# Performance work log

Measured on AMD Instinct MI355X. Metric: run time of the kernel, lower is better.

The kernel has to match this reference:

```python
import jax, jax.numpy as jnp
import numpy as np
from jax.scipy.linalg import expm

U_SHAPE = (4, 32, 16, 16, 16, 3, 3)   # [mu, t, x, y, z, 3, 3]
W_SHAPE = (8, 32, 16, 16, 16, 3, 3)   # [feature, t, x, y, z, 3, 3]


def setup_inputs() -> dict:
    key = jax.random.key(0)
    k = jax.random.split(key, 5)
    return {
        "U_re": jax.random.normal(k[0], U_SHAPE, jnp.float32),
        "U_im": jax.random.normal(k[1], U_SHAPE, jnp.float32),
        "W_re": jax.random.normal(k[2], W_SHAPE, jnp.float32),
        "W_im": jax.random.normal(k[3], W_SHAPE, jnp.float32),
        "ah_weights": jax.random.normal(k[4], (4, W_SHAPE[0]), jnp.float32),
    }


def reference(U_re, U_im, W_re, W_im, ah_weights):
    U = (U_re + 1j * U_im).astype(jnp.complex64)
    W = (W_re + 1j * W_im).astype(jnp.complex64)

    # anti-hermitian part: W - W^dagger
    W_adj = jnp.conj(jnp.swapaxes(W, -1, -2))
    A = W - W_adj
    # traceless projection
    tr = jnp.trace(A, axis1=-2, axis2=-1)  # [i,t,x,y,z]
    A = A - (tr / 3.0)[..., None, None] * jnp.eye(3, dtype=A.dtype)

    # exponent: (1j*w) contracted with (-1j*A) == w contracted with A
    E = jnp.einsum('ui,itxyzab->utxyzab', ah_weights.astype(A.dtype), A)

    # batched 3x3 matrix exponential over the whole lattice
    E_flat = E.reshape(-1, 3, 3)
    expE = jax.vmap(expm)(E_flat).reshape(E.shape)

    # apply to gauge links: exp(...) @ U
    return jnp.einsum('utxyzij,utxyzjk->utxyzik', expE, U)
```

## Files before the change

kernel.cpp:

```cpp
#include <hip/hip_runtime.h>
#include <math.h>

#define NSITES 131072

struct cplx { float re, im; };

__device__ __forceinline__ cplx cadd(cplx a, cplx b) { return {a.re + b.re, a.im + b.im}; }
__device__ __forceinline__ cplx csub(cplx a, cplx b) { return {a.re - b.re, a.im - b.im}; }
__device__ __forceinline__ cplx cmul(cplx a, cplx b) {
    return { fmaf(a.re, b.re, -(a.im * b.im)), fmaf(a.re, b.im, a.im * b.re) };
}
__device__ __forceinline__ cplx cmadd(cplx a, cplx b, cplx c) {
    return { fmaf(a.re, b.re, fmaf(-a.im, b.im, c.re)),
             fmaf(a.re, b.im, fmaf( a.im, b.re, c.im)) };
}
__device__ __forceinline__ cplx cscale(cplx a, float s) { return {a.re * s, a.im * s}; }

struct __attribute__((aligned(4))) f3 { float x, y, z; };
__device__ __forceinline__ void ld9(const float* __restrict__ p, float* r) {
    f3 a = *(const f3*)p, b = *(const f3*)(p + 3), c = *(const f3*)(p + 6);
    r[0] = a.x; r[1] = a.y; r[2] = a.z;
    r[3] = b.x; r[4] = b.y; r[5] = b.z;
    r[6] = c.x; r[7] = c.y; r[8] = c.z;
}

#define GLDS(g, l) __builtin_amdgcn_global_load_lds( \
    (const __attribute__((address_space(1))) void*)(g), \
    (__attribute__((address_space(3))) void*)(l), 16, 0, 0)

__global__ __launch_bounds__(256, 4) void lge_exp_kernel(
    const float* __restrict__ U_re, const float* __restrict__ U_im,
    const float* __restrict__ W_re, const float* __restrict__ W_im,
    const float* __restrict__ ahw,  float* __restrict__ out)
{
    __shared__ __align__(16) float Wl[4 * 2304];

    const int tid   = threadIdx.x;
    const int w     = tid >> 6;
    const int lane  = tid & 63;
    const int site0 = blockIdx.x << 6;

    {
        const char* baseRe = (const char*)W_re;
        const char* baseIm = (const char*)W_im;
        float* ldst = Wl + w * 2304 + ((16 * 64) / 4) * 0;
        #pragma unroll
        for (int k = 0; k < 9; k++) {
            int p   = k * 64 + lane;
            int c   = p / 36;
            int off = (p - c * 36) * 16;
            int f   = c & 7;
            const char* gb = (c < 8) ? baseRe : baseIm;
            const char* g  = gb + (size_t)((f * NSITES + site0 + 16 * w)) * 36 + off;
            GLDS(g, (char*)(Wl + w * 2304) + k * 1024);
        }
    }
    asm volatile("" ::: "memory");
    __builtin_amdgcn_s_waitcnt(0);
    asm volatile("" ::: "memory");

    const int siteL = lane >> 2;
    const int mu    = lane & 3;
    const int gsite = site0 + 16 * w + siteL;

    const float4* ahw4 = (const float4*)ahw;
    float4 wlo = ahw4[mu * 2], whi = ahw4[mu * 2 + 1];
    const float wfv[8] = { wlo.x, wlo.y, wlo.z, wlo.w, whi.x, whi.y, whi.z, whi.w };

    const int ub = (mu * NSITES + gsite) * 9;
    float ur[9], ui[9];
    ld9(U_re + ub, ur);
    ld9(U_im + ub, ui);

    const float* wre = Wl + w * 2304 + siteL * 9;
    const float* wim = wre + 8 * 144;
    cplx E[9];
    #pragma unroll
    for (int m = 0; m < 9; m++) E[m] = {0.f, 0.f};

    #pragma unroll
    for (int f = 0; f < 8; f++) {
        float wr[9], wi[9];
        #pragma unroll
        for (int m = 0; m < 9; m++) { wr[m] = wre[f * 144 + m]; wi[m] = wim[f * 144 + m]; }

        float Ar[9], Ai[9];
        #pragma unroll
        for (int a = 0; a < 3; a++)
            #pragma unroll
            for (int b = 0; b < 3; b++) {
                int ab = 3 * a + b, ba = 3 * b + a;
                Ar[ab] = wr[ab] - wr[ba];
                Ai[ab] = wi[ab] + wi[ba];
            }
        float t3 = (Ai[0] + Ai[4] + Ai[8]) * (1.f / 3.f);
        Ai[0] -= t3; Ai[4] -= t3; Ai[8] -= t3;

        const float wf = wfv[f];
        #pragma unroll
        for (int m = 0; m < 9; m++) {
            E[m].re = fmaf(wf, Ar[m], E[m].re);
            E[m].im = fmaf(wf, Ai[m], E[m].im);
        }
    }

    cplx p = {0.f, 0.f};
    #pragma unroll
    for (int a = 0; a < 3; a++)
        #pragma unroll
        for (int b = 0; b < 3; b++)
            p = cmadd(E[3 * a + b], E[3 * b + a], p);
    p = cscale(p, 0.5f);

    cplx q = csub(cmul(E[0], csub(cmul(E[4], E[8]), cmul(E[5], E[7]))),
                  cmul(E[1], csub(cmul(E[3], E[8]), cmul(E[5], E[6]))));
    q = cadd(q, cmul(E[2], csub(cmul(E[3], E[7]), cmul(E[4], E[6]))));

    float r2 = 0.f;
    #pragma unroll
    for (int m = 0; m < 9; m++)
        r2 = fmaf(E[m].re, E[m].re, fmaf(E[m].im, E[m].im, r2));
    float rn = sqrtf(r2);

    int sc = 0;
    if (rn > 0.5f) sc = (int)ceilf(log2f(rn * 2.0f));
    sc = min(max(sc, 0), 40);
    float inv  = exp2f(-(float)sc);
    float inv2 = inv * inv;
    cplx pX = cscale(p, inv2);
    cplx qX = cscale(q, inv2 * inv);

    cplx T0 = {1.f, 0.f}, T1 = {0.f, 0.f}, T2 = {0.f, 0.f};
    cplx S0 = {1.f, 0.f}, S1 = {0.f, 0.f}, S2 = {0.f, 0.f};
    #pragma unroll
    for (int n = 1; n <= 10; n++) {
        float rcp = 1.0f / (float)n;
        cplx nT0 = cscale(cmul(T2, qX), rcp);
        cplx nT1 = cscale(cmadd(T2, pX, T0), rcp);
        cplx nT2 = cscale(T1, rcp);
        T0 = nT0; T1 = nT1; T2 = nT2;
        S0 = cadd(S0, T0); S1 = cadd(S1, T1); S2 = cadd(S2, T2);
    }

    for (int k = 0; k < sc; k++) {
        cplx f0 = S0, f1 = S1, f2 = S2;
        cplx f12 = cmul(f1, f2);
        cplx f22 = cmul(f2, f2);
        S0 = cmadd(cscale(f12, 2.f), qX, cmul(f0, f0));
        S1 = cmadd(f22, qX, cmadd(cscale(f12, 2.f), pX, cscale(cmul(f0, f1), 2.f)));
        S2 = cmadd(f22, pX, cadd(cscale(cmul(f0, f2), 2.f), cmul(f1, f1)));
    }
    cplx g0 = S0;
    cplx g1 = cscale(S1, inv);
    cplx g2 = cscale(S2, inv2);

    cplx Um[9];
    #pragma unroll
    for (int m = 0; m < 9; m++) Um[m] = { ur[m], ui[m] };

    cplx V[9];
    #pragma unroll
    for (int a = 0; a < 3; a++)
        #pragma unroll
        for (int b = 0; b < 3; b++) {
            cplx acc = cmul(E[3 * a], Um[b]);
            acc = cmadd(E[3 * a + 1], Um[3 + b], acc);
            acc = cmadd(E[3 * a + 2], Um[6 + b], acc);
            V[3 * a + b] = acc;
        }

    float o[9];
    #pragma unroll
    for (int a = 0; a < 3; a++)
        #pragma unroll
        for (int b = 0; b < 3; b++) {
            cplx z = cmul(E[3 * a], V[b]);
            z = cmadd(E[3 * a + 1], V[3 + b], z);
            z = cmadd(E[3 * a + 2], V[6 + b], z);
            cplx oc = cmul(g0, Um[3 * a + b]);
            oc = cmadd(g1, V[3 * a + b], oc);
            oc = cmadd(g2, z, oc);
            o[3 * a + b] = oc.re;
        }

    float* ob = out + ub;
    *(f3*)(ob)     = { o[0], o[1], o[2] };
    *(f3*)(ob + 3) = { o[3], o[4], o[5] };
    *(f3*)(ob + 6) = { o[6], o[7], o[8] };
}

extern "C" void kernel_launch(void* const* d_in, const int* in_sizes, int n_in,
                              void* d_out, int out_size, void* d_ws, size_t ws_size,
                              hipStream_t stream) {
    const float* U_re = (const float*)d_in[0];
    const float* U_im = (const float*)d_in[1];
    const float* W_re = (const float*)d_in[2];
    const float* W_im = (const float*)d_in[3];
    const float* ahw  = (const float*)d_in[4];
    float* out = (float*)d_out;
    lge_exp_kernel<<<dim3(NSITES / 64), dim3(256), 0, stream>>>(
        U_re, U_im, W_re, W_im, ahw, out);
}
```

Measured before the change: 147.6 us.

## Exploit anti-Hermitian structure, stage W re/im in halved LDS, raise occupancy

Uses the anti-Hermitian traceless structure of E to compute only the independent entries (real off-diagonals from W_re and imaginary parts from W_im). The trace-squared term is obtained from the Frobenius norm and the determinant from a real Hermitian formula, so the Cayley-Hamilton coefficients become purely real or purely imaginary and the series and squaring loops simplify. W_re and W_im are staged one after the other through a single LDS slab half the previous size, with partial 4-byte loads, which allows launch bounds to rise to 8 blocks per CU. The aim is fewer FLOPs and registers and more waves in flight, at the cost of serialising the two W loads and relying on the exact symmetry of E.

Result: slower. 209.1 us (+41.6%).

```diff
diff --git a/kernel.cpp b/kernel.cpp
--- a/kernel.cpp
+++ b/kernel.cpp
@@ -6,15 +6,9 @@
 struct cplx { float re, im; };
 
 __device__ __forceinline__ cplx cadd(cplx a, cplx b) { return {a.re + b.re, a.im + b.im}; }
-__device__ __forceinline__ cplx csub(cplx a, cplx b) { return {a.re - b.re, a.im - b.im}; }
 __device__ __forceinline__ cplx cmul(cplx a, cplx b) {
     return { fmaf(a.re, b.re, -(a.im * b.im)), fmaf(a.re, b.im, a.im * b.re) };
 }
-__device__ __forceinline__ cplx cmadd(cplx a, cplx b, cplx c) {
-    return { fmaf(a.re, b.re, fmaf(-a.im, b.im, c.re)),
-             fmaf(a.re, b.im, fmaf( a.im, b.re, c.im)) };
-}
-__device__ __forceinline__ cplx cscale(cplx a, float s) { return {a.re * s, a.im * s}; }
 
 struct __attribute__((aligned(4))) f3 { float x, y, z; };
 __device__ __forceinline__ void ld9(const float* __restrict__ p, float* r) {
@@ -24,164 +18,179 @@
     r[6] = c.x; r[7] = c.y; r[8] = c.z;
 }
 
-#define GLDS(g, l) __builtin_amdgcn_global_load_lds( \
+#define GLDS16(g, l) __builtin_amdgcn_global_load_lds( \
     (const __attribute__((address_space(1))) void*)(g), \
     (__attribute__((address_space(3))) void*)(l), 16, 0, 0)
-
-__global__ __launch_bounds__(256, 4) void lge_exp_kernel(
+#define GLDS4(g, l) __builtin_amdgcn_global_load_lds( \
+    (const __attribute__((address_space(1))) void*)(g), \
+    (__attribute__((address_space(3))) void*)(l), 4, 0, 0)
+
+__device__ __forceinline__ void stage_slab(const char* __restrict__ base,
+                                           char* lds, int wsite, int lane)
+{
+    #pragma unroll
+    for (int k = 0; k < 4; k++) {
+        int p   = k * 64 + lane;
+        int c   = p / 36;
+        int off = (p - c * 36) * 16;
+        const char* g = base + (size_t)(c * NSITES + wsite) * 36 + off;
+        GLDS16(g, lds + k * 1024);
+    }
+    #pragma unroll
+    for (int k = 0; k < 2; k++) {
+        int off = 64 + 4 * (k * 64 + lane);
+        const char* g = base + (size_t)(7 * NSITES + wsite) * 36 + off;
+        GLDS4(g, lds + 4096 + k * 256);
+    }
+}
+
+#define ECOL(m0, m1, m2, v0, v1, v2) do { \
+    v0.re = fmaf(-ed0, m0.im, fmaf(er01, m1.re, fmaf(-ei01, m1.im, fmaf(er02, m2.re, -(ei02 * m2.im))))); \
+    v0.im = fmaf( ed0, m0.re, fmaf(er01, m1.im, fmaf( ei01, m1.re, fmaf(er02, m2.im,  (ei02 * m2.re))))); \
+    v1.re = fmaf(-er01, m0.re, fmaf(-ei01, m0.im, fmaf(-ed1, m1.im, fmaf(er12, m2.re, -(ei12 * m2.im))))); \
+    v1.im = fmaf(-er01, m0.im, fmaf( ei01, m0.re, fmaf( ed1, m1.re, fmaf(er12, m2.im,  (ei12 * m2.re))))); \
+    v2.re = fmaf(-er02, m0.re, fmaf(-ei02, m0.im, fmaf(-er12, m1.re, fmaf(-ei12, m1.im, -(ed2 * m2.im))))); \
+    v2.im = fmaf(-er02, m0.im, fmaf( ei02, m0.re, fmaf(-er12, m1.im, fmaf( ei12, m1.re,  (ed2 * m2.re))))); \
+} while (0)
+
+#define OCOMB(m, v, z) \
+    fmaf(g0.re, m.re, fmaf(-g0.im, m.im, fmaf(g1.re, v.re, fmaf(-g1.im, v.im, \
+    fmaf(g2.re, z.re, -(g2.im * z.im))))))
+
+__global__ __launch_bounds__(256, 8) void lge_exp_kernel(
     const float* __restrict__ U_re, const float* __restrict__ U_im,
     const float* __restrict__ W_re, const float* __restrict__ W_im,
     const float* __restrict__ ahw,  float* __restrict__ out)
 {
-    __shared__ __align__(16) float Wl[4 * 2304];
+    __shared__ __align__(16) float Wl[4 * 1152];
 
     const int tid   = threadIdx.x;
     const int w     = tid >> 6;
     const int lane  = tid & 63;
     const int site0 = blockIdx.x << 6;
-
-    {
-        const char* baseRe = (const char*)W_re;
-        const char* baseIm = (const char*)W_im;
-        float* ldst = Wl + w * 2304 + ((16 * 64) / 4) * 0;
-        #pragma unroll
-        for (int k = 0; k < 9; k++) {
-            int p   = k * 64 + lane;
-            int c   = p / 36;
-            int off = (p - c * 36) * 16;
-            int f   = c & 7;
-            const char* gb = (c < 8) ? baseRe : baseIm;
-            const char* g  = gb + (size_t)((f * NSITES + site0 + 16 * w)) * 36 + off;
-            GLDS(g, (char*)(Wl + w * 2304) + k * 1024);
-        }
-    }
-    asm volatile("" ::: "memory");
-    __builtin_amdgcn_s_waitcnt(0);
-    asm volatile("" ::: "memory");
+    const int wsite = site0 + 16 * w;
+
+    float* ldsw = Wl + w * 1152;
+
+    stage_slab((const char*)W_re, (char*)ldsw, wsite, lane);
 
     const int siteL = lane >> 2;
     const int mu    = lane & 3;
-    const int gsite = site0 + 16 * w + siteL;
+    const int gsite = wsite + siteL;
 
     const float4* ahw4 = (const float4*)ahw;
     float4 wlo = ahw4[mu * 2], whi = ahw4[mu * 2 + 1];
     const float wfv[8] = { wlo.x, wlo.y, wlo.z, wlo.w, whi.x, whi.y, whi.z, whi.w };
+
+    asm volatile("" ::: "memory");
+    __builtin_amdgcn_s_waitcnt(0);
+    asm volatile("" ::: "memory");
+
+    const float* wp = ldsw + siteL * 9;
+    float er01 = 0.f, er02 = 0.f, er12 = 0.f;
+    #pragma unroll
+    for (int f = 0; f < 8; f++) {
+        const float* r = wp + f * 144;
+        float wf = wfv[f];
+        er01 = fmaf(wf, r[1] - r[3], er01);
+        er02 = fmaf(wf, r[2] - r[6], er02);
+        er12 = fmaf(wf, r[5] - r[7], er12);
+    }
+
+    asm volatile("s_waitcnt lgkmcnt(0)" ::: "memory");
+
+    stage_slab((const char*)W_im, (char*)ldsw, wsite, lane);
 
     const int ub = (mu * NSITES + gsite) * 9;
     float ur[9], ui[9];
     ld9(U_re + ub, ur);
     ld9(U_im + ub, ui);
 
-    const float* wre = Wl + w * 2304 + siteL * 9;
-    const float* wim = wre + 8 * 144;
-    cplx E[9];
-    #pragma unroll
-    for (int m = 0; m < 9; m++) E[m] = {0.f, 0.f};
-
+    asm volatile("" ::: "memory");
+    __builtin_amdgcn_s_waitcnt(0);
+    asm volatile("" ::: "memory");
+
+    float a0=0.f,a1=0.f,a2=0.f,a3=0.f,a4=0.f,a5=0.f,a6=0.f,a7=0.f,a8=0.f;
     #pragma unroll
     for (int f = 0; f < 8; f++) {
-        float wr[9], wi[9];
-        #pragma unroll
-        for (int m = 0; m < 9; m++) { wr[m] = wre[f * 144 + m]; wi[m] = wim[f * 144 + m]; }
-
-        float Ar[9], Ai[9];
-        #pragma unroll
-        for (int a = 0; a < 3; a++)
-            #pragma unroll
-            for (int b = 0; b < 3; b++) {
-                int ab = 3 * a + b, ba = 3 * b + a;
-                Ar[ab] = wr[ab] - wr[ba];
-                Ai[ab] = wi[ab] + wi[ba];
-            }
-        float t3 = (Ai[0] + Ai[4] + Ai[8]) * (1.f / 3.f);
-        Ai[0] -= t3; Ai[4] -= t3; Ai[8] -= t3;
-
-        const float wf = wfv[f];
-        #pragma unroll
-        for (int m = 0; m < 9; m++) {
-            E[m].re = fmaf(wf, Ar[m], E[m].re);
-            E[m].im = fmaf(wf, Ai[m], E[m].im);
-        }
-    }
-
-    cplx p = {0.f, 0.f};
-    #pragma unroll
-    for (int a = 0; a < 3; a++)
-        #pragma unroll
-        for (int b = 0; b < 3; b++)
-            p = cmadd(E[3 * a + b], E[3 * b + a], p);
-    p = cscale(p, 0.5f);
-
-    cplx q = csub(cmul(E[0], csub(cmul(E[4], E[8]), cmul(E[5], E[7]))),
-                  cmul(E[1], csub(cmul(E[3], E[8]), cmul(E[5], E[6]))));
-    q = cadd(q, cmul(E[2], csub(cmul(E[3], E[7]), cmul(E[4], E[6]))));
-
-    float r2 = 0.f;
-    #pragma unroll
-    for (int m = 0; m < 9; m++)
-        r2 = fmaf(E[m].re, E[m].re, fmaf(E[m].im, E[m].im, r2));
-    float rn = sqrtf(r2);
-
-    int sc = 0;
-    if (rn > 0.5f) sc = (int)ceilf(log2f(rn * 2.0f));
-    sc = min(max(sc, 0), 40);
-    float inv  = exp2f(-(float)sc);
-    float inv2 = inv * inv;
-    cplx pX = cscale(p, inv2);
-    cplx qX = cscale(q, inv2 * inv);
+        const float* r = wp + f * 144;
+        float wf = wfv[f];
+        a0 = fmaf(wf, r[0], a0); a1 = fmaf(wf, r[1], a1); a2 = fmaf(wf, r[2], a2);
+        a3 = fmaf(wf, r[3], a3); a4 = fmaf(wf, r[4], a4); a5 = fmaf(wf, r[5], a5);
+        a6 = fmaf(wf, r[6], a6); a7 = fmaf(wf, r[7], a7); a8 = fmaf(wf, r[8], a8);
+    }
+    const float ei01 = a1 + a3, ei02 = a2 + a6, ei12 = a5 + a7;
+    const float t3  = (a0 + a4 + a8) * (2.f / 3.f);
+    const float ed0 = fmaf(2.f, a0, -t3);
+    const float ed1 = fmaf(2.f, a4, -t3);
+    const float ed2 = fmaf(2.f, a8, -t3);
+
+    float r2 = fmaf(er01, er01, fmaf(er02, er02, fmaf(er12, er12,
+               fmaf(ei01, ei01, fmaf(ei02, ei02, ei12 * ei12)))));
+    r2 = fmaf(2.f, r2, fmaf(ed0, ed0, fmaf(ed1, ed1, ed2 * ed2)));
+
+    const float n01 = fmaf(ei01, ei01, er01 * er01);
+    const float n02 = fmaf(ei02, ei02, er02 * er02);
+    const float n12 = fmaf(ei12, ei12, er12 * er12);
+    const float zre = fmaf(ei01, ei12, -(er01 * er12));
+    const float zim = -fmaf(ei01, er12, er01 * ei12);
+    const float detH = ed0 * ed1 * ed2
+                     + 2.f * fmaf(zre, ei02, -(zim * er02))
+                     - fmaf(ed0, n12, fmaf(ed1, n02, ed2 * n01));
+
+    int e; (void)frexpf(r2, &e);
+    int sc = (e <= -2) ? 0 : min(1 + ((e + 1) >> 1), 40);
+    const float inv  = __int_as_float((127 - sc) << 23);
+    const float inv2 = inv * inv;
+    const float px   = -0.5f * r2 * inv2;
+    const float qxi  = -detH * (inv2 * inv);
 
     cplx T0 = {1.f, 0.f}, T1 = {0.f, 0.f}, T2 = {0.f, 0.f};
     cplx S0 = {1.f, 0.f}, S1 = {0.f, 0.f}, S2 = {0.f, 0.f};
     #pragma unroll
     for (int n = 1; n <= 10; n++) {
-        float rcp = 1.0f / (float)n;
-        cplx nT0 = cscale(cmul(T2, qX), rcp);
-        cplx nT1 = cscale(cmadd(T2, pX, T0), rcp);
-        cplx nT2 = cscale(T1, rcp);
+        float c  = 1.f / (float)n;
+        float qc = qxi * c;
+        cplx nT0 = { -qc * T2.im, qc * T2.re };
+        cplx nT1 = { c * fmaf(px, T2.re, T0.re), c * fmaf(px, T2.im, T0.im) };
+        cplx nT2 = { c * T1.re, c * T1.im };
         T0 = nT0; T1 = nT1; T2 = nT2;
         S0 = cadd(S0, T0); S1 = cadd(S1, T1); S2 = cadd(S2, T2);
     }
 
+    const float q2 = 2.f * qxi;
     for (int k = 0; k < sc; k++) {
         cplx f0 = S0, f1 = S1, f2 = S2;
         cplx f12 = cmul(f1, f2);
-        cplx f22 = cmul(f2, f2);
-        S0 = cmadd(cscale(f12, 2.f), qX, cmul(f0, f0));
-        S1 = cmadd(f22, qX, cmadd(cscale(f12, 2.f), pX, cscale(cmul(f0, f1), 2.f)));
-        S2 = cmadd(f22, pX, cadd(cscale(cmul(f0, f2), 2.f), cmul(f1, f1)));
-    }
-    cplx g0 = S0;
-    cplx g1 = cscale(S1, inv);
-    cplx g2 = cscale(S2, inv2);
-
-    cplx Um[9];
-    #pragma unroll
-    for (int m = 0; m < 9; m++) Um[m] = { ur[m], ui[m] };
-
-    cplx V[9];
-    #pragma unroll
-    for (int a = 0; a < 3; a++)
-        #pragma unroll
-        for (int b = 0; b < 3; b++) {
-            cplx acc = cmul(E[3 * a], Um[b]);
-            acc = cmadd(E[3 * a + 1], Um[3 + b], acc);
-            acc = cmadd(E[3 * a + 2], Um[6 + b], acc);
-            V[3 * a + b] = acc;
-        }
+        cplx f01 = cmul(f0, f1);
+        cplx f02 = cmul(f0, f2);
+        float f00re = fmaf(f0.re, f0.re, -(f0.im * f0.im)), f00im = 2.f * f0.re * f0.im;
+        float f11re = fmaf(f1.re, f1.re, -(f1.im * f1.im)), f11im = 2.f * f1.re * f1.im;
+        float f22re = fmaf(f2.re, f2.re, -(f2.im * f2.im)), f22im = 2.f * f2.re * f2.im;
+        S0.re = fmaf(-q2, f12.im, f00re);
+        S0.im = fmaf( q2, f12.re, f00im);
+        S1.re = fmaf(-qxi, f22im, 2.f * fmaf(px, f12.re, f01.re));
+        S1.im = fmaf( qxi, f22re, 2.f * fmaf(px, f12.im, f01.im));
+        S2.re = fmaf(px, f22re, fmaf(2.f, f02.re, f11re));
+        S2.im = fmaf(px, f22im, fmaf(2.f, f02.im, f11im));
+    }
+    const cplx g0 = S0;
+    const cplx g1 = { S1.re * inv,  S1.im * inv  };
+    const cplx g2 = { S2.re * inv2, S2.im * inv2 };
 
     float o[9];
     #pragma unroll
-    for (int a = 0; a < 3; a++)
-        #pragma unroll
-        for (int b = 0; b < 3; b++) {
-            cplx z = cmul(E[3 * a], V[b]);
-            z = cmadd(E[3 * a + 1], V[3 + b], z);
-            z = cmadd(E[3 * a + 2], V[6 + b], z);
-            cplx oc = cmul(g0, Um[3 * a + b]);
-            oc = cmadd(g1, V[3 * a + b], oc);
-            oc = cmadd(g2, z, oc);
-            o[3 * a + b] = oc.re;
-        }
+    for (int b = 0; b < 3; b++) {
+        cplx m0 = { ur[b],     ui[b]     };
+        cplx m1 = { ur[3 + b], ui[3 + b] };
+        cplx m2 = { ur[6 + b], ui[6 + b] };
+        cplx v0, v1, v2, z0, z1, z2;
+        ECOL(m0, m1, m2, v0, v1, v2);
+        ECOL(v0, v1, v2, z0, z1, z2);
+        o[b]     = OCOMB(m0, v0, z0);
+        o[3 + b] = OCOMB(m1, v1, z1);
+        o[6 + b] = OCOMB(m2, v2, z2);
+    }
 
     float* ob = out + ub;
     *(f3*)(ob)     = { o[0], o[1], o[2] };
```
